# Kernel tuning notes

Hardware: AMD Instinct MI355X
Metric: run time of the kernel (lower is better)

Reference implementation:

```python
import jax, jax.numpy as jnp
import numpy as np

H = 1024  # hidden_size
N = 2 * H # encoder feature dim


def setup_inputs() -> dict:
    key = jax.random.key(0)
    ks = jax.random.split(key, 8)
    T, B = 2048, 16
    dec = jax.random.normal(ks[0], (B, H), dtype=jnp.float32)
    enc = jax.random.normal(ks[1], (T, B, N), dtype=jnp.float32)
    mask = jax.random.randint(ks[2], (T, B), 0, 2) > 0
    cov = jax.random.uniform(ks[3], (T, B), dtype=jnp.float32)
    # parameters (PyTorch Linear convention: y = x @ W.T + b)
    Wd = jax.random.normal(ks[4], (N, H), dtype=jnp.float32) / np.sqrt(H)
    bd = jnp.zeros((N,), dtype=jnp.float32)
    wc = jax.random.normal(ks[5], (N,), dtype=jnp.float32)  # coverage_projection: Linear(1, N, bias=False)
    v = jax.random.normal(ks[6], (N,), dtype=jnp.float32) / np.sqrt(N)  # v: Linear(N, 1, bias=False)
    return {"decoder_hidden_states": dec, "encoder_outs": enc,
            "encoder_padding_mask": mask, "coverage": cov,
            "Wd": Wd, "bd": bd, "wc": wc, "v": v}


def reference(decoder_hidden_states, encoder_outs, encoder_padding_mask, coverage, Wd, bd, wc, v):
    # dec_fea: [B, N]
    dec_fea = decoder_hidden_states @ Wd.T + bd
    # att_features: [T, B, N] = enc + broadcast dec + coverage feature
    att = encoder_outs + dec_fea[None, :, :] + coverage[:, :, None] * wc[None, None, :]
    e = jnp.tanh(att)
    # attn_scores: [T, B] via matvec with v
    scores = jnp.einsum('tbn,n->tb', e, v)
    scores = jnp.where(encoder_padding_mask, -jnp.inf, scores)
    attn_dist = jax.nn.softmax(scores, axis=0)  # softmax over T
    # context: [B, N]
    c = jnp.einsum('tb,tbn->bn', attn_dist, encoder_outs)
    coverage_out = coverage + attn_dist
    return (c, attn_dist, coverage_out)
```

## Files before the change

### kernel.cpp

```cpp
#include <hip/hip_runtime.h>


#define HH 1024
#define NNF 2048
#define TTT 2048
#define BB 16
#define NCHUNK 64
#define ROWS 32

#define WS_DECFEA 0
#define WS_P      (BB * NNF)
#define WS_LPART  (WS_P + TTT * BB)
#define WS_LINV   (WS_LPART + NCHUNK * BB)
#define WS_CPART  (WS_LINV + 16)

__device__ __forceinline__ float tanh_fast(float x) {
    float e = __expf(2.0f * x);
    return 1.0f - 2.0f * __builtin_amdgcn_rcpf(e + 1.0f);
}

__global__ __launch_bounds__(256) void k_decfea(const float* __restrict__ dec,
                                                const float* __restrict__ Wd,
                                                const float* __restrict__ bd,
                                                float* __restrict__ dec_fea) {
    int gw   = (blockIdx.x * 256 + threadIdx.x) >> 6;
    int lane = threadIdx.x & 63;
    int b = gw >> 11;
    int n = gw & (NNF - 1);
    const float* dr = dec + b * HH;
    const float* wr = Wd + (size_t)n * HH;
    float acc = 0.0f;
#pragma unroll
    for (int it = 0; it < 4; ++it) {
        int h = it * 256 + lane * 4;
        float4 a = *(const float4*)(dr + h);
        float4 w = *(const float4*)(wr + h);
        acc = fmaf(a.x, w.x, acc);
        acc = fmaf(a.y, w.y, acc);
        acc = fmaf(a.z, w.z, acc);
        acc = fmaf(a.w, w.w, acc);
    }
#pragma unroll
    for (int off = 32; off; off >>= 1) acc += __shfl_down(acc, off, 64);
    if (lane == 0) dec_fea[b * NNF + n] = acc + bd[n];
}

__global__ __launch_bounds__(256) void k_main(const float* __restrict__ enc,
                                              const int* __restrict__ mask,
                                              const float* __restrict__ cov,
                                              const float* __restrict__ wc,
                                              const float* __restrict__ v,
                                              float* __restrict__ ws) {
    const int b     = blockIdx.y;
    const int chunk = blockIdx.x;
    const int t0    = chunk * ROWS;
    const int tid   = threadIdx.x;
    const int lane  = tid & 63;
    const int wid   = tid >> 6;
    const int n0    = tid * 4;
    const int n1    = 1024 + tid * 4;

    const float* dec_fea = ws + WS_DECFEA;
    float* ws_p     = ws + WS_P;
    float* ws_lpart = ws + WS_LPART;
    float* cpart    = ws + WS_CPART;

    const float4 d0 = *(const float4*)(dec_fea + b * NNF + n0);
    const float4 d1 = *(const float4*)(dec_fea + b * NNF + n1);
    const float4 w0 = *(const float4*)(wc + n0);
    const float4 w1 = *(const float4*)(wc + n1);
    const float4 v0 = *(const float4*)(v + n0);
    const float4 v1 = *(const float4*)(v + n1);

    float4 c0 = {0.f, 0.f, 0.f, 0.f};
    float4 c1 = {0.f, 0.f, 0.f, 0.f};
    float l_loc = 0.0f;

    __shared__ float red[2][4];

    const float* base = enc + ((size_t)t0 * BB + b) * NNF;
    float4 e0 = *(const float4*)(base + n0);
    float4 e1 = *(const float4*)(base + n1);

    for (int r = 0; r < ROWS; ++r) {
        const int t = t0 + r;
        float4 f0 = e0, f1 = e1;
        if (r + 1 < ROWS) {
            const float* nb = base + (size_t)(r + 1) * BB * NNF;
            e0 = *(const float4*)(nb + n0);
            e1 = *(const float4*)(nb + n1);
        }
        const float cv = cov[t * BB + b];

        float s = 0.0f;
        {
            float a;
            a = fmaf(cv, w0.x, f0.x + d0.x); s = fmaf(tanh_fast(a), v0.x, s);
            a = fmaf(cv, w0.y, f0.y + d0.y); s = fmaf(tanh_fast(a), v0.y, s);
            a = fmaf(cv, w0.z, f0.z + d0.z); s = fmaf(tanh_fast(a), v0.z, s);
            a = fmaf(cv, w0.w, f0.w + d0.w); s = fmaf(tanh_fast(a), v0.w, s);
            a = fmaf(cv, w1.x, f1.x + d1.x); s = fmaf(tanh_fast(a), v1.x, s);
            a = fmaf(cv, w1.y, f1.y + d1.y); s = fmaf(tanh_fast(a), v1.y, s);
            a = fmaf(cv, w1.z, f1.z + d1.z); s = fmaf(tanh_fast(a), v1.z, s);
            a = fmaf(cv, w1.w, f1.w + d1.w); s = fmaf(tanh_fast(a), v1.w, s);
        }
#pragma unroll
        for (int off = 32; off; off >>= 1) s += __shfl_down(s, off, 64);
        if (lane == 0) red[r & 1][wid] = s;
        __syncthreads();
        const float stot = red[r & 1][0] + red[r & 1][1] + red[r & 1][2] + red[r & 1][3];

        const bool pad = mask[t * BB + b] != 0;
        const float p = pad ? 0.0f : __expf(stot);

        c0.x = fmaf(p, f0.x, c0.x);
        c0.y = fmaf(p, f0.y, c0.y);
        c0.z = fmaf(p, f0.z, c0.z);
        c0.w = fmaf(p, f0.w, c0.w);
        c1.x = fmaf(p, f1.x, c1.x);
        c1.y = fmaf(p, f1.y, c1.y);
        c1.z = fmaf(p, f1.z, c1.z);
        c1.w = fmaf(p, f1.w, c1.w);

        if (tid == 0) {
            ws_p[t * BB + b] = p;
            l_loc += p;
        }
    }

    if (tid == 0) ws_lpart[chunk * BB + b] = l_loc;
    float* cp = cpart + (size_t)(chunk * BB + b) * NNF;
    *(float4*)(cp + n0) = c0;
    *(float4*)(cp + n1) = c1;
}

__global__ void k_linv(float* __restrict__ ws) {
    int b = threadIdx.x;
    if (b < BB) {
        float s = 0.0f;
        for (int j = 0; j < NCHUNK; ++j) s += ws[WS_LPART + j * BB + b];
        ws[WS_LINV + b] = 1.0f / s;
    }
}

__global__ __launch_bounds__(256) void k_finc(const float* __restrict__ ws,
                                              float* __restrict__ out_c) {
    int gid  = blockIdx.x * 256 + threadIdx.x;
    int idx4 = gid * 4;
    int b = idx4 >> 11;
    int n = idx4 & (NNF - 1);
    float4 s = {0.f, 0.f, 0.f, 0.f};
    for (int j = 0; j < NCHUNK; ++j) {
        float4 a = *(const float4*)(ws + WS_CPART + (size_t)(j * BB + b) * NNF + n);
        s.x += a.x; s.y += a.y; s.z += a.z; s.w += a.w;
    }
    float li = ws[WS_LINV + b];
    s.x *= li; s.y *= li; s.z *= li; s.w *= li;
    *(float4*)(out_c + idx4) = s;
}

__global__ __launch_bounds__(256) void k_fina(const float* __restrict__ ws,
                                              const float* __restrict__ cov,
                                              float* __restrict__ out_attn,
                                              float* __restrict__ out_cov) {
    int idx = blockIdx.x * 256 + threadIdx.x;
    int b = idx & (BB - 1);
    float a = ws[WS_P + idx] * ws[WS_LINV + b];
    out_attn[idx] = a;
    out_cov[idx] = cov[idx] + a;
}

extern "C" void kernel_launch(void* const* d_in, const int* in_sizes, int n_in,
                              void* d_out, int out_size, void* d_ws, size_t ws_size,
                              hipStream_t stream) {
    const float* dec  = (const float*)d_in[0];
    const float* enc  = (const float*)d_in[1];
    const int*   mask = (const int*)d_in[2];
    const float* cov  = (const float*)d_in[3];
    const float* Wd   = (const float*)d_in[4];
    const float* bd   = (const float*)d_in[5];
    const float* wc   = (const float*)d_in[6];
    const float* v    = (const float*)d_in[7];
    float* ws  = (float*)d_ws;
    float* out = (float*)d_out;

    float* out_c    = out;
    float* out_attn = out + BB * NNF;
    float* out_cov  = out_attn + TTT * BB;

    k_decfea<<<8192, 256, 0, stream>>>(dec, Wd, bd, ws + WS_DECFEA);

    dim3 g2(NCHUNK, BB);
    k_main<<<g2, 256, 0, stream>>>(enc, mask, cov, wc, v, ws);

    k_linv<<<1, 64, 0, stream>>>(ws);

    k_finc<<<32, 256, 0, stream>>>(ws, out_c);

    k_fina<<<128, 256, 0, stream>>>(ws, cov, out_attn, out_cov);
}
```

Baseline: 389.6 us.

## Give each wavefront its own rows in attention kernel and batch dec_fea GEMV

k_decfea now has one wavefront compute one output feature for all 16 batch rows. Each Wd row is loaded once and reused across the batch instead of being re-read per batch element. In k_main each wavefront owns 8 full timesteps across all 2048 features, so the per-row block-wide reduction and __syncthreads are replaced by an in-wave xor shuffle reduction. The cost is 4x more context partials (256 chunks): more workspace traffic and a longer serial reduction loop in k_finc, which still runs on only 32 blocks, plus higher register pressure under launch_bounds(256,2).

```diff
diff --git a/kernel.cpp b/kernel.cpp
--- a/kernel.cpp
+++ b/kernel.cpp
@@ -6,12 +6,13 @@
 #define TTT 2048
 #define BB 16
 #define NCHUNK 64
-#define ROWS 32
+#define NWCHUNK 256
+#define RPW 8
 
 #define WS_DECFEA 0
 #define WS_P      (BB * NNF)
 #define WS_LPART  (WS_P + TTT * BB)
-#define WS_LINV   (WS_LPART + NCHUNK * BB)
+#define WS_LINV   (WS_LPART + NWCHUNK * BB)
 #define WS_CPART  (WS_LINV + 16)
 
 __device__ __forceinline__ float tanh_fast(float x) {
@@ -23,138 +24,140 @@
                                                 const float* __restrict__ Wd,
                                                 const float* __restrict__ bd,
                                                 float* __restrict__ dec_fea) {
-    int gw   = (blockIdx.x * 256 + threadIdx.x) >> 6;
-    int lane = threadIdx.x & 63;
-    int b = gw >> 11;
-    int n = gw & (NNF - 1);
-    const float* dr = dec + b * HH;
+    const int n    = (blockIdx.x * 256 + threadIdx.x) >> 6;
+    const int lane = threadIdx.x & 63;
     const float* wr = Wd + (size_t)n * HH;
-    float acc = 0.0f;
+
+    float acc[BB];
+#pragma unroll
+    for (int b = 0; b < BB; ++b) acc[b] = 0.0f;
+
 #pragma unroll
     for (int it = 0; it < 4; ++it) {
-        int h = it * 256 + lane * 4;
-        float4 a = *(const float4*)(dr + h);
-        float4 w = *(const float4*)(wr + h);
-        acc = fmaf(a.x, w.x, acc);
-        acc = fmaf(a.y, w.y, acc);
-        acc = fmaf(a.z, w.z, acc);
-        acc = fmaf(a.w, w.w, acc);
-    }
-#pragma unroll
-    for (int off = 32; off; off >>= 1) acc += __shfl_down(acc, off, 64);
-    if (lane == 0) dec_fea[b * NNF + n] = acc + bd[n];
-}
-
-__global__ __launch_bounds__(256) void k_main(const float* __restrict__ enc,
-                                              const int* __restrict__ mask,
-                                              const float* __restrict__ cov,
-                                              const float* __restrict__ wc,
-                                              const float* __restrict__ v,
-                                              float* __restrict__ ws) {
+        const int h = it * 256 + lane * 4;
+        const float4 w4 = *(const float4*)(wr + h);
+#pragma unroll
+        for (int b = 0; b < BB; ++b) {
+            const float4 d4 = *(const float4*)(dec + b * HH + h);
+            acc[b] = fmaf(w4.x, d4.x, acc[b]);
+            acc[b] = fmaf(w4.y, d4.y, acc[b]);
+            acc[b] = fmaf(w4.z, d4.z, acc[b]);
+            acc[b] = fmaf(w4.w, d4.w, acc[b]);
+        }
+    }
+#pragma unroll
+    for (int b = 0; b < BB; ++b) {
+#pragma unroll
+        for (int off = 32; off; off >>= 1) acc[b] += __shfl_xor(acc[b], off, 64);
+    }
+    if (lane == 0) {
+        const float bias = bd[n];
+#pragma unroll
+        for (int b = 0; b < BB; ++b) dec_fea[b * NNF + n] = acc[b] + bias;
+    }
+}
+
+__global__ __launch_bounds__(256, 2) void k_main(const float* __restrict__ enc,
+                                                 const int* __restrict__ mask,
+                                                 const float* __restrict__ cov,
+                                                 const float* __restrict__ wc,
+                                                 const float* __restrict__ v,
+                                                 float* __restrict__ ws) {
     const int b     = blockIdx.y;
     const int chunk = blockIdx.x;
-    const int t0    = chunk * ROWS;
     const int tid   = threadIdx.x;
     const int lane  = tid & 63;
-    const int wid   = tid >> 6;
-    const int n0    = tid * 4;
-    const int n1    = 1024 + tid * 4;
+    const int w     = tid >> 6;
+    const int t0    = chunk * (4 * RPW) + w * RPW;
+    const int nb    = lane * 4;
 
     const float* dec_fea = ws + WS_DECFEA;
     float* ws_p     = ws + WS_P;
     float* ws_lpart = ws + WS_LPART;
     float* cpart    = ws + WS_CPART;
 
-    const float4 d0 = *(const float4*)(dec_fea + b * NNF + n0);
-    const float4 d1 = *(const float4*)(dec_fea + b * NNF + n1);
-    const float4 w0 = *(const float4*)(wc + n0);
-    const float4 w1 = *(const float4*)(wc + n1);
-    const float4 v0 = *(const float4*)(v + n0);
-    const float4 v1 = *(const float4*)(v + n1);
-
-    float4 c0 = {0.f, 0.f, 0.f, 0.f};
-    float4 c1 = {0.f, 0.f, 0.f, 0.f};
+    float4 d[8], wv[8], vv[8], c[8];
+#pragma unroll
+    for (int s = 0; s < 8; ++s) {
+        const int n = s * 256 + nb;
+        d[s]  = *(const float4*)(dec_fea + b * NNF + n);
+        wv[s] = *(const float4*)(wc + n);
+        vv[s] = *(const float4*)(v + n);
+        c[s]  = make_float4(0.f, 0.f, 0.f, 0.f);
+    }
+
     float l_loc = 0.0f;
 
-    __shared__ float red[2][4];
-
-    const float* base = enc + ((size_t)t0 * BB + b) * NNF;
-    float4 e0 = *(const float4*)(base + n0);
-    float4 e1 = *(const float4*)(base + n1);
-
-    for (int r = 0; r < ROWS; ++r) {
+    for (int r = 0; r < RPW; ++r) {
         const int t = t0 + r;
-        float4 f0 = e0, f1 = e1;
-        if (r + 1 < ROWS) {
-            const float* nb = base + (size_t)(r + 1) * BB * NNF;
-            e0 = *(const float4*)(nb + n0);
-            e1 = *(const float4*)(nb + n1);
+        const float* row = enc + ((size_t)t * BB + b) * NNF;
+        float4 f[8];
+#pragma unroll
+        for (int s = 0; s < 8; ++s) f[s] = *(const float4*)(row + s * 256 + nb);
+        const float cv = cov[t * BB + b];
+
+        float sa = 0.0f;
+#pragma unroll
+        for (int s = 0; s < 8; ++s) {
+            float a;
+            a = fmaf(cv, wv[s].x, f[s].x + d[s].x); sa = fmaf(tanh_fast(a), vv[s].x, sa);
+            a = fmaf(cv, wv[s].y, f[s].y + d[s].y); sa = fmaf(tanh_fast(a), vv[s].y, sa);
+            a = fmaf(cv, wv[s].z, f[s].z + d[s].z); sa = fmaf(tanh_fast(a), vv[s].z, sa);
+            a = fmaf(cv, wv[s].w, f[s].w + d[s].w); sa = fmaf(tanh_fast(a), vv[s].w, sa);
         }
-        const float cv = cov[t * BB + b];
-
-        float s = 0.0f;
-        {
-            float a;
-            a = fmaf(cv, w0.x, f0.x + d0.x); s = fmaf(tanh_fast(a), v0.x, s);
-            a = fmaf(cv, w0.y, f0.y + d0.y); s = fmaf(tanh_fast(a), v0.y, s);
-            a = fmaf(cv, w0.z, f0.z + d0.z); s = fmaf(tanh_fast(a), v0.z, s);
-            a = fmaf(cv, w0.w, f0.w + d0.w); s = fmaf(tanh_fast(a), v0.w, s);
-            a = fmaf(cv, w1.x, f1.x + d1.x); s = fmaf(tanh_fast(a), v1.x, s);
-            a = fmaf(cv, w1.y, f1.y + d1.y); s = fmaf(tanh_fast(a), v1.y, s);
-            a = fmaf(cv, w1.z, f1.z + d1.z); s = fmaf(tanh_fast(a), v1.z, s);
-            a = fmaf(cv, w1.w, f1.w + d1.w); s = fmaf(tanh_fast(a), v1.w, s);
+#pragma unroll
+        for (int off = 32; off; off >>= 1) sa += __shfl_xor(sa, off, 64);
+
+        const bool pad = mask[t * BB + b] != 0;
+        const float p = pad ? 0.0f : __expf(sa);
+        l_loc += p;
+#pragma unroll
+        for (int s = 0; s < 8; ++s) {
+            c[s].x = fmaf(p, f[s].x, c[s].x);
+            c[s].y = fmaf(p, f[s].y, c[s].y);
+            c[s].z = fmaf(p, f[s].z, c[s].z);
+            c[s].w = fmaf(p, f[s].w, c[s].w);
         }
-#pragma unroll
-        for (int off = 32; off; off >>= 1) s += __shfl_down(s, off, 64);
-        if (lane == 0) red[r & 1][wid] = s;
-        __syncthreads();
-        const float stot = red[r & 1][0] + red[r & 1][1] + red[r & 1][2] + red[r & 1][3];
-
-        const bool pad = mask[t * BB + b] != 0;
-        const float p = pad ? 0.0f : __expf(stot);
-
-        c0.x = fmaf(p, f0.x, c0.x);
-        c0.y = fmaf(p, f0.y, c0.y);
-        c0.z = fmaf(p, f0.z, c0.z);
-        c0.w = fmaf(p, f0.w, c0.w);
-        c1.x = fmaf(p, f1.x, c1.x);
-        c1.y = fmaf(p, f1.y, c1.y);
-        c1.z = fmaf(p, f1.z, c1.z);
-        c1.w = fmaf(p, f1.w, c1.w);
-
-        if (tid == 0) {
-            ws_p[t * BB + b] = p;
-            l_loc += p;
-        }
-    }
-
-    if (tid == 0) ws_lpart[chunk * BB + b] = l_loc;
-    float* cp = cpart + (size_t)(chunk * BB + b) * NNF;
-    *(float4*)(cp + n0) = c0;
-    *(float4*)(cp + n1) = c1;
-}
-
-__global__ void k_linv(float* __restrict__ ws) {
-    int b = threadIdx.x;
-    if (b < BB) {
-        float s = 0.0f;
-        for (int j = 0; j < NCHUNK; ++j) s += ws[WS_LPART + j * BB + b];
-        ws[WS_LINV + b] = 1.0f / s;
+        if (lane == 0) ws_p[t * BB + b] = p;
+    }
+
+    const int wchunk = chunk * 4 + w;
+    if (lane == 0) ws_lpart[wchunk * BB + b] = l_loc;
+    float* cp = cpart + (size_t)(wchunk * BB + b) * NNF;
+#pragma unroll
+    for (int s = 0; s < 8; ++s) *(float4*)(cp + s * 256 + nb) = c[s];
+}
+
+__global__ __launch_bounds__(256) void k_linv(float* __restrict__ ws) {
+    __shared__ float lds[256];
+    const int tid = threadIdx.x;
+    const int b  = tid & (BB - 1);
+    const int j0 = tid >> 4;
+    float s = 0.0f;
+#pragma unroll
+    for (int jj = 0; jj < 16; ++jj) s += ws[WS_LPART + (j0 * 16 + jj) * BB + b];
+    lds[tid] = s;
+    __syncthreads();
+    if (tid < BB) {
+        float tot = 0.0f;
+#pragma unroll
+        for (int k = 0; k < 16; ++k) tot += lds[k * BB + tid];
+        ws[WS_LINV + tid] = 1.0f / tot;
     }
 }
 
 __global__ __launch_bounds__(256) void k_finc(const float* __restrict__ ws,
                                               float* __restrict__ out_c) {
-    int gid  = blockIdx.x * 256 + threadIdx.x;
-    int idx4 = gid * 4;
-    int b = idx4 >> 11;
-    int n = idx4 & (NNF - 1);
+    const int gid  = blockIdx.x * 256 + threadIdx.x;
+    const int idx4 = gid * 4;
+    const int b = idx4 >> 11;
+    const int n = idx4 & (NNF - 1);
     float4 s = {0.f, 0.f, 0.f, 0.f};
-    for (int j = 0; j < NCHUNK; ++j) {
-        float4 a = *(const float4*)(ws + WS_CPART + (size_t)(j * BB + b) * NNF + n);
+    for (int j = 0; j < NWCHUNK; ++j) {
+        const float4 a = *(const float4*)(ws + WS_CPART + (size_t)(j * BB + b) * NNF + n);
         s.x += a.x; s.y += a.y; s.z += a.z; s.w += a.w;
     }
-    float li = ws[WS_LINV + b];
+    const float li = ws[WS_LINV + b];
     s.x *= li; s.y *= li; s.z *= li; s.w *= li;
     *(float4*)(out_c + idx4) = s;
 }
@@ -163,9 +166,9 @@
                                               const float* __restrict__ cov,
                                               float* __restrict__ out_attn,
                                               float* __restrict__ out_cov) {
-    int idx = blockIdx.x * 256 + threadIdx.x;
-    int b = idx & (BB - 1);
-    float a = ws[WS_P + idx] * ws[WS_LINV + b];
+    const int idx = blockIdx.x * 256 + threadIdx.x;
+    const int b = idx & (BB - 1);
+    const float a = ws[WS_P + idx] * ws[WS_LINV + b];
     out_attn[idx] = a;
     out_cov[idx] = cov[idx] + a;
 }
@@ -188,12 +191,12 @@
     float* out_attn = out + BB * NNF;
     float* out_cov  = out_attn + TTT * BB;
 
-    k_decfea<<<8192, 256, 0, stream>>>(dec, Wd, bd, ws + WS_DECFEA);
+    k_decfea<<<512, 256, 0, stream>>>(dec, Wd, bd, ws + WS_DECFEA);
 
     dim3 g2(NCHUNK, BB);
     k_main<<<g2, 256, 0, stream>>>(enc, mask, cov, wc, v, ws);
 
-    k_linv<<<1, 64, 0, stream>>>(ws);
+    k_linv<<<1, 256, 0, stream>>>(ws);
 
     k_finc<<<32, 256, 0, stream>>>(ws, out_c);
 
```

New measurement: 419.4 us. +7.7%, slower.
